# Kernel optimization log

Measured on AMD Instinct MI355X. Metric: run time of the kernel, lower is better.

## Reference

```python
import jax, jax.numpy as jnp
import numpy as np


def setup_inputs() -> dict:
    key = jax.random.key(0)
    ks = jax.random.split(key, 5)
    B, C, H, W = 32, 32, 64, 64   # latent feature map (latent_space_channel_dim=32)
    D, K = 32, 512                # quant_dim, codebook_size
    return {
        "z": jax.random.normal(ks[0], (B, C, H, W), jnp.float32),
        "quant_w": jax.random.normal(ks[1], (D, C), jnp.float32) * 0.1,   # 1x1 conv kernel
        "quant_b": jnp.zeros((D,), jnp.float32),
        "codebook": jax.random.normal(ks[2], (K, D), jnp.float32),
        "post_quant_w": jax.random.normal(ks[3], (C, D), jnp.float32) * 0.1,
        "post_quant_b": jnp.zeros((C,), jnp.float32),
    }


def reference(z, quant_w, quant_b, codebook, post_quant_w, post_quant_b):
    B, C, H, W = z.shape
    D = quant_w.shape[0]
    # quant_conv: 1x1 conv == channel GEMM
    x = jnp.einsum('bchw,dc->bdhw', z, quant_w) + quant_b[None, :, None, None]
    # rearrange 'b c h w -> b c (h w)' then flatten tokens to [B*HW, D]
    xf = x.transpose(0, 2, 3, 1).reshape(-1, D)
    # squared euclidean distances to codebook (cdist**2), argmin, gather
    d2 = (jnp.sum(xf * xf, axis=-1, keepdims=True)
          - 2.0 * (xf @ codebook.T)
          + jnp.sum(codebook * codebook, axis=-1)[None, :])  # [B*HW, K]
    idx = jnp.argmin(d2, axis=-1)                              # [B*HW]
    q = codebook[idx]                                          # gather [B*HW, D]
    # commitment loss (encoder pull) + codebook loss (learnable codebook, no EMA)
    commit = jnp.mean((jax.lax.stop_gradient(q) - xf) ** 2)
    cb_loss = jnp.mean((q - jax.lax.stop_gradient(xf)) ** 2)
    loss = commit + cb_loss
    # straight-through estimator
    q_st = xf + jax.lax.stop_gradient(q - xf)
    qmap = q_st.reshape(B, H, W, D).transpose(0, 3, 1, 2)      # 'b c (h w) -> b c h w'
    # post_quant_conv: 1x1 conv back to latent channels
    out = jnp.einsum('bdhw,cd->bchw', qmap, post_quant_w) + post_quant_b[None, :, None, None]
    return out, idx.reshape(B, H * W), loss
```

## Files before the change

### kernel.cpp

```cpp
#include <hip/hip_runtime.h>

#define C_    32
#define D_    32
#define K_    512
#define HW_   4096
#define NTOK  131072
#define IDX_OFF   4194304
#define LOSS_OFF  4325376
#define TAU   2e-4f

#define WS_CBN   0
#define WS_CBHF  4096
#define WS_CBLF  36864
#define WS_LOSSP 69632
#define WS_NEEDED 86016

typedef __attribute__((ext_vector_type(8))) _Float16 f16x8;
typedef __attribute__((ext_vector_type(8))) short    short8;
typedef __attribute__((ext_vector_type(4))) float    f32x4;

#define WAVE_FENCE() do { asm volatile("s_waitcnt lgkmcnt(0)" ::: "memory"); \
                          __builtin_amdgcn_sched_barrier(0); } while (0)

__device__ inline short f2h_hi(float v, float* rest) {
    const _Float16 h = (_Float16)v;
    *rest = v - (float)h;
    return __builtin_bit_cast(short, h);
}

__global__ __launch_bounds__(256)
void prep_cb(const float* __restrict__ cb, float* __restrict__ cbn,
             short* __restrict__ cbhf, short* __restrict__ cblf)
{
    const int k = blockIdx.x * 256 + threadIdx.x;
    const int nt = k >> 4, lr = k & 15;
    const float* row = cb + k * D_;
    float s = 0.f;
    short h[32], lo[32];
    #pragma unroll
    for (int d = 0; d < D_; ++d) {
        const float v = row[d]; s = fmaf(v, v, s);
        float r; h[d] = f2h_hi(v, &r);
        lo[d] = __builtin_bit_cast(short, (_Float16)r);
    }
    cbn[k] = s;
    #pragma unroll
    for (int j = 0; j < 4; ++j) {
        *(short8*)(cbhf + nt * 512 + (j * 16 + lr) * 8) = *(const short8*)(h  + 8 * j);
        *(short8*)(cblf + nt * 512 + (j * 16 + lr) * 8) = *(const short8*)(lo + 8 * j);
    }
}

__global__ __launch_bounds__(512, 2)
void vq_fused(const float* __restrict__ z,  const float* __restrict__ qw,
              const float* __restrict__ qb, const float* __restrict__ cb,
              const float* __restrict__ pw, const float* __restrict__ pb,
              const short* __restrict__ cbhf, const short* __restrict__ cblf,
              const float* __restrict__ cbn, float* __restrict__ lossp,
              float* __restrict__ out)
{
    __shared__ __align__(16) short cbh_s[16384];
    __shared__ __align__(16) short cbl_s[16384];
    __shared__ float cbn_s[K_];
    __shared__ float xsh[8][32][33];
    __shared__ int   sidx[8][32];

    const int tid = threadIdx.x;
    const int wv = tid >> 6, l = tid & 63;

    #pragma unroll
    for (int i = 0; i < 4; ++i)
        ((float4*)cbh_s)[tid + 512 * i] = ((const float4*)cbhf)[tid + 512 * i];
    #pragma unroll
    for (int i = 0; i < 4; ++i)
        ((float4*)cbl_s)[tid + 512 * i] = ((const float4*)cblf)[tid + 512 * i];
    if (tid < K_) cbn_s[tid] = cbn[tid];
    __syncthreads();

    const int T0 = (blockIdx.x * 8 + wv) * 32;
    const int b = T0 >> 12, hw0 = T0 & (HW_ - 1);
    const int tok = l & 31, half = l >> 5;

    {
        const float* zbase = z + (size_t)b * (C_ * HW_) + hw0 + tok;
        float zv[C_];
        #pragma unroll
        for (int c = 0; c < C_; ++c) zv[c] = zbase[(size_t)c * HW_];
        const int d0 = half * 16;
        #pragma unroll
        for (int i = 0; i < 16; ++i) {
            float a = qb[d0 + i];
            const float4* qr = (const float4*)(qw + (d0 + i) * C_);
            #pragma unroll
            for (int c4 = 0; c4 < 8; ++c4) {
                const float4 q4 = qr[c4];
                a = fmaf(zv[4*c4+0], q4.x, a); a = fmaf(zv[4*c4+1], q4.y, a);
                a = fmaf(zv[4*c4+2], q4.z, a); a = fmaf(zv[4*c4+3], q4.w, a);
            }
            xsh[wv][tok][d0 + i] = a;
        }
    }
    WAVE_FENCE();

    const int lr = l & 15, lg = l >> 4;
    short8 sh0, sl0, sh1, sl1;
    #pragma unroll
    for (int j = 0; j < 8; ++j) {
        float r0, r1;
        sh0[j] = f2h_hi(xsh[wv][lr][lg * 8 + j], &r0);
        sl0[j] = __builtin_bit_cast(short, (_Float16)r0);
        sh1[j] = f2h_hi(xsh[wv][16 + lr][lg * 8 + j], &r1);
        sl1[j] = __builtin_bit_cast(short, (_Float16)r1);
    }
    const f16x8 ah0 = __builtin_bit_cast(f16x8, sh0);
    const f16x8 al0 = __builtin_bit_cast(f16x8, sl0);
    const f16x8 ah1 = __builtin_bit_cast(f16x8, sh1);
    const f16x8 al1 = __builtin_bit_cast(f16x8, sl1);

    float b1[8], b2[8]; int i1[8];
    #pragma unroll
    for (int s = 0; s < 8; ++s) { b1[s] = 3.4e38f; b2[s] = 3.4e38f; i1[s] = 0; }

    #pragma unroll 2
    for (int nt = 0; nt < 32; ++nt) {
        const f16x8 bh = __builtin_bit_cast(f16x8, *(const short8*)(cbh_s + nt * 512 + l * 8));
        const f16x8 bl = __builtin_bit_cast(f16x8, *(const short8*)(cbl_s + nt * 512 + l * 8));
        const float cn = cbn_s[nt * 16 + lr];
        f32x4 acc0 = {0.f,0.f,0.f,0.f}, acc1 = {0.f,0.f,0.f,0.f};
        acc0 = __builtin_amdgcn_mfma_f32_16x16x32_f16(ah0, bh, acc0, 0, 0, 0);
        acc0 = __builtin_amdgcn_mfma_f32_16x16x32_f16(ah0, bl, acc0, 0, 0, 0);
        acc0 = __builtin_amdgcn_mfma_f32_16x16x32_f16(al0, bh, acc0, 0, 0, 0);
        acc1 = __builtin_amdgcn_mfma_f32_16x16x32_f16(ah1, bh, acc1, 0, 0, 0);
        acc1 = __builtin_amdgcn_mfma_f32_16x16x32_f16(ah1, bl, acc1, 0, 0, 0);
        acc1 = __builtin_amdgcn_mfma_f32_16x16x32_f16(al1, bh, acc1, 0, 0, 0);
        const int n = nt * 16 + lr;
        #pragma unroll
        for (int r = 0; r < 4; ++r) {
            {
                const float d2 = fmaf(-2.f, acc0[r], cn);
                const bool lt1 = d2 < b1[r], lt2 = d2 < b2[r];
                b2[r] = lt1 ? b1[r] : (lt2 ? d2 : b2[r]);
                b1[r] = lt1 ? d2 : b1[r];
                i1[r] = lt1 ? n  : i1[r];
            }
            {
                const float d2 = fmaf(-2.f, acc1[r], cn);
                const bool lt1 = d2 < b1[4+r], lt2 = d2 < b2[4+r];
                b2[4+r] = lt1 ? b1[4+r] : (lt2 ? d2 : b2[4+r]);
                b1[4+r] = lt1 ? d2 : b1[4+r];
                i1[4+r] = lt1 ? n  : i1[4+r];
            }
        }
    }
    #pragma unroll
    for (int mk = 1; mk < 16; mk <<= 1) {
        #pragma unroll
        for (int s = 0; s < 8; ++s) {
            const float ob1 = __shfl_xor(b1[s], mk);
            const int   oi1 = __shfl_xor(i1[s], mk);
            const float ob2 = __shfl_xor(b2[s], mk);
            const bool take = (ob1 < b1[s]) || (ob1 == b1[s] && oi1 < i1[s]);
            const float loser = take ? b1[s] : ob1;
            b1[s] = take ? ob1 : b1[s];
            i1[s] = take ? oi1 : i1[s];
            b2[s] = fminf(fminf(b2[s], ob2), loser);
        }
    }
    #pragma unroll
    for (int s = 0; s < 8; ++s) {
        if (lr == s) {
            const int tokW = (s >> 2) * 16 + lg * 4 + (s & 3);
            sidx[wv][tokW] = i1[s] | (((b2[s] - b1[s]) < TAU) ? 512 : 0);
        }
    }
    WAVE_FENCE();

    {
        const int sv = sidx[wv][tok];
        unsigned long long m = __ballot((l < 32) && (sv & 512));
        while (m) {
            const int j = __ffsll(m) - 1; m &= m - 1;
            float xfj[D_];
            #pragma unroll
            for (int d = 0; d < D_; ++d) xfj[d] = xsh[wv][j][d];
            float bb = 3.4e38f; int bi = 0;
            #pragma unroll
            for (int p = 0; p < 8; ++p) {
                const int c = l + 64 * p;
                const float* row = cb + (size_t)c * D_;
                float p0 = 0.f, p1 = 0.f, p2 = 0.f, p3 = 0.f;
                #pragma unroll
                for (int d = 0; d < D_; d += 4) {
                    p0 = fmaf(xfj[d],   row[d],   p0); p1 = fmaf(xfj[d+1], row[d+1], p1);
                    p2 = fmaf(xfj[d+2], row[d+2], p2); p3 = fmaf(xfj[d+3], row[d+3], p3);
                }
                const float dd = fmaf(-2.f, (p0 + p1) + (p2 + p3), cbn_s[c]);
                if (dd < bb) { bb = dd; bi = c; }
            }
            #pragma unroll
            for (int s = 1; s < 64; s <<= 1) {
                const float ob = __shfl_xor(bb, s); const int oi = __shfl_xor(bi, s);
                if (ob < bb || (ob == bb && oi < bi)) { bb = ob; bi = oi; }
            }
            if (l == j) sidx[wv][j] = bi;
        }
    }
    WAVE_FENCE();
    const int myidx = sidx[wv][tok] & 511;

    if (l < 32) out[IDX_OFF + T0 + l] = (float)(sidx[wv][l] & 511);

    float qreg[16];
    {
        const float4* qrow = (const float4*)(cb + (size_t)myidx * D_ + half * 16);
        #pragma unroll
        for (int d4 = 0; d4 < 4; ++d4) {
            const float4 t = qrow[d4];
            qreg[4*d4+0] = t.x; qreg[4*d4+1] = t.y; qreg[4*d4+2] = t.z; qreg[4*d4+3] = t.w;
        }
    }
    float lacc = 0.f;
    #pragma unroll
    for (int i = 0; i < 16; ++i) {
        const float df = qreg[i] - xsh[wv][tok][half * 16 + i];
        lacc = fmaf(df, df, lacc);
    }
    lacc += __shfl_down(lacc, 32);
    lacc += __shfl_down(lacc, 16); lacc += __shfl_down(lacc, 8);
    lacc += __shfl_down(lacc, 4);  lacc += __shfl_down(lacc, 2);
    lacc += __shfl_down(lacc, 1);
    if (l == 0) lossp[blockIdx.x * 8 + wv] = lacc;

    #pragma unroll
    for (int i = 0; i < 16; ++i) xsh[wv][tok][half * 16 + i] = qreg[i];
    WAVE_FENCE();

    {
        const int c0 = half * 16;
        float a[16];
        #pragma unroll
        for (int i = 0; i < 16; ++i) a[i] = pb[c0 + i];
        #pragma unroll
        for (int d4 = 0; d4 < 8; ++d4) {
            const float q0 = xsh[wv][tok][d4*4+0], q1 = xsh[wv][tok][d4*4+1];
            const float q2 = xsh[wv][tok][d4*4+2], q3 = xsh[wv][tok][d4*4+3];
            #pragma unroll
            for (int i = 0; i < 16; ++i) {
                const float4 p4 = *(const float4*)(pw + (c0 + i) * D_ + d4 * 4);
                a[i] = fmaf(q0, p4.x, a[i]); a[i] = fmaf(q1, p4.y, a[i]);
                a[i] = fmaf(q2, p4.z, a[i]); a[i] = fmaf(q3, p4.w, a[i]);
            }
        }
        float* obase = out + (size_t)b * (C_ * HW_) + hw0 + tok;
        #pragma unroll
        for (int i = 0; i < 16; ++i) obase[(size_t)(c0 + i) * HW_] = a[i];
    }
}

__global__ __launch_bounds__(256)
void loss_final(const float* __restrict__ lossp, float* __restrict__ out)
{
    __shared__ float lsum[4];
    const int tid = threadIdx.x;
    float s = 0.f;
    for (int i = tid; i < 4096; i += 256) s += lossp[i];
    s += __shfl_down(s, 32); s += __shfl_down(s, 16);
    s += __shfl_down(s, 8);  s += __shfl_down(s, 4);
    s += __shfl_down(s, 2);  s += __shfl_down(s, 1);
    const int wv = tid >> 6, l = tid & 63;
    if (l == 0) lsum[wv] = s;
    __syncthreads();
    if (tid == 0)
        out[LOSS_OFF] = ((lsum[0] + lsum[1]) + (lsum[2] + lsum[3])) * (2.0f / (float)(NTOK * D_));
}

__global__ __launch_bounds__(256)
void vq_mono(const float* __restrict__ z,  const float* __restrict__ qw,
             const float* __restrict__ qb, const float* __restrict__ cb,
             const float* __restrict__ pw, const float* __restrict__ pb,
             float* __restrict__ out)
{
    __shared__ float cbn_s[K_];
    __shared__ float lsum[4];
    const int tid = threadIdx.x;
    for (int k = tid; k < K_; k += 256) {
        const float* row = cb + k * D_;
        float s = 0.f;
        #pragma unroll
        for (int d = 0; d < D_; ++d) s = fmaf(row[d], row[d], s);
        cbn_s[k] = s;
    }
    __syncthreads();
    const int token = blockIdx.x * 256 + tid;
    const int b = token >> 12, hw = token & (HW_ - 1);
    const float* zbase = z + (size_t)b * C_ * HW_ + hw;
    float zv[C_];
    #pragma unroll
    for (int c = 0; c < C_; ++c) zv[c] = zbase[(size_t)c * HW_];
    float xf[D_];
    #pragma unroll
    for (int d = 0; d < D_; ++d) {
        float a = qb[d];
        #pragma unroll
        for (int c = 0; c < C_; ++c) a = fmaf(zv[c], qw[d * C_ + c], a);
        xf[d] = a;
    }
    float best = 3.4e38f; int bi = 0;
    #pragma unroll 2
    for (int k = 0; k < K_; ++k) {
        const float* row = cb + k * D_;
        float p0 = 0.f, p1 = 0.f, p2 = 0.f, p3 = 0.f;
        #pragma unroll
        for (int d = 0; d < D_; d += 4) {
            p0 = fmaf(xf[d+0], row[d+0], p0); p1 = fmaf(xf[d+1], row[d+1], p1);
            p2 = fmaf(xf[d+2], row[d+2], p2); p3 = fmaf(xf[d+3], row[d+3], p3);
        }
        const float s = fmaf(-2.f, (p0+p1)+(p2+p3), cbn_s[k]);
        if (s < best) { best = s; bi = k; }
    }
    out[IDX_OFF + token] = (float)bi;
    const float* qrow = cb + (size_t)bi * D_;
    float qv[D_];
    #pragma unroll
    for (int d = 0; d < D_; ++d) qv[d] = qrow[d];
    float l = 0.f;
    #pragma unroll
    for (int d = 0; d < D_; ++d) { const float df = qv[d] - xf[d]; l = fmaf(df, df, l); }
    float* obase = out + (size_t)b * C_ * HW_ + hw;
    #pragma unroll
    for (int c = 0; c < C_; ++c) {
        float a = pb[c];
        #pragma unroll
        for (int d = 0; d < D_; ++d) a = fmaf(qv[d], pw[c * D_ + d], a);
        obase[(size_t)c * HW_] = a;
    }
    #pragma unroll
    for (int off = 32; off; off >>= 1) l += __shfl_down(l, off);
    const int wid = tid >> 6, lane = tid & 63;
    if (lane == 0) lsum[wid] = l;
    __syncthreads();
    if (tid == 0) {
        const float t = (lsum[0] + lsum[1]) + (lsum[2] + lsum[3]);
        atomicAdd(out + LOSS_OFF, t * (2.0f / (float)(NTOK * D_)));
    }
}

extern "C" void kernel_launch(void* const* d_in, const int* in_sizes, int n_in,
                              void* d_out, int out_size, void* d_ws, size_t ws_size,
                              hipStream_t stream) {
    (void)in_sizes; (void)n_in; (void)out_size;
    const float* z  = (const float*)d_in[0];
    const float* qw = (const float*)d_in[1];
    const float* qb = (const float*)d_in[2];
    const float* cb = (const float*)d_in[3];
    const float* pw = (const float*)d_in[4];
    const float* pb = (const float*)d_in[5];
    float* out = (float*)d_out;

    if (ws_size < (size_t)WS_NEEDED) {
        hipMemsetAsync((char*)d_out + (size_t)LOSS_OFF * sizeof(float), 0, sizeof(float), stream);
        vq_mono<<<NTOK / 256, 256, 0, stream>>>(z, qw, qb, cb, pw, pb, out);
        return;
    }
    char* ws = (char*)d_ws;
    float* cbn   = (float*)(ws + WS_CBN);
    short* cbhf  = (short*)(ws + WS_CBHF);
    short* cblf  = (short*)(ws + WS_CBLF);
    float* lossp = (float*)(ws + WS_LOSSP);

    prep_cb<<<2, 256, 0, stream>>>(cb, cbn, cbhf, cblf);
    vq_fused<<<512, 512, 0, stream>>>(z, qw, qb, cb, pw, pb, cbhf, cblf, cbn, lossp, out);
    loss_final<<<1, 256, 0, stream>>>(lossp, out);
}
```

Measured before the change: 81.87 us.

## Keep projected tokens in MFMA register layout, pack argmin index into distance bits

The quant-conv output is now computed directly in the per-lane MFMA A-operand layout, so the xsh shared-memory staging buffer is dropped. Argmin tracking packs the candidate index into the low 9 mantissa bits of the distance and uses fminf/fmaxf, which removes the separate index registers and compares. Occupancy is raised to 4 blocks per CU, block IDs are swizzled, and the post-conv is restructured so each wave writes 64 contiguous tokens. The truncated distances force a much larger ambiguity threshold, which sends more tokens through the exact fp32 fallback path.

New measurement: 121.5 us. 1.48x slower.

```diff
diff --git a/kernel.cpp b/kernel.cpp
--- a/kernel.cpp
+++ b/kernel.cpp
@@ -7,7 +7,7 @@
 #define NTOK  131072
 #define IDX_OFF   4194304
 #define LOSS_OFF  4325376
-#define TAU   2e-4f
+#define TAU   1.6e-2f
 
 #define WS_CBN   0
 #define WS_CBHF  4096
@@ -21,12 +21,6 @@
 
 #define WAVE_FENCE() do { asm volatile("s_waitcnt lgkmcnt(0)" ::: "memory"); \
                           __builtin_amdgcn_sched_barrier(0); } while (0)
-
-__device__ inline short f2h_hi(float v, float* rest) {
-    const _Float16 h = (_Float16)v;
-    *rest = v - (float)h;
-    return __builtin_bit_cast(short, h);
-}
 
 __global__ __launch_bounds__(256)
 void prep_cb(const float* __restrict__ cb, float* __restrict__ cbn,
@@ -40,8 +34,9 @@
     #pragma unroll
     for (int d = 0; d < D_; ++d) {
         const float v = row[d]; s = fmaf(v, v, s);
-        float r; h[d] = f2h_hi(v, &r);
-        lo[d] = __builtin_bit_cast(short, (_Float16)r);
+        const _Float16 hh = (_Float16)v;
+        h[d]  = __builtin_bit_cast(short, hh);
+        lo[d] = __builtin_bit_cast(short, (_Float16)(v - (float)hh));
     }
     cbn[k] = s;
     #pragma unroll
@@ -51,7 +46,7 @@
     }
 }
 
-__global__ __launch_bounds__(512, 2)
+__global__ __launch_bounds__(512, 4)
 void vq_fused(const float* __restrict__ z,  const float* __restrict__ qw,
               const float* __restrict__ qb, const float* __restrict__ cb,
               const float* __restrict__ pw, const float* __restrict__ pb,
@@ -62,11 +57,11 @@
     __shared__ __align__(16) short cbh_s[16384];
     __shared__ __align__(16) short cbl_s[16384];
     __shared__ float cbn_s[K_];
-    __shared__ float xsh[8][32][33];
     __shared__ int   sidx[8][32];
 
     const int tid = threadIdx.x;
     const int wv = tid >> 6, l = tid & 63;
+    const int lr = l & 15, lg = l >> 4;
 
     #pragma unroll
     for (int i = 0; i < 4; ++i)
@@ -77,51 +72,56 @@
     if (tid < K_) cbn_s[tid] = cbn[tid];
     __syncthreads();
 
-    const int T0 = (blockIdx.x * 8 + wv) * 32;
+    const int bid = blockIdx.x;
+    const int swz = (bid & 7) * 64 + (bid >> 3);
+    const int T0 = swz * 256;
     const int b = T0 >> 12, hw0 = T0 & (HW_ - 1);
-    const int tok = l & 31, half = l >> 5;
-
+    const int hwW = hw0 + wv * 32;
+
+    float a0[8], a1[8];
     {
-        const float* zbase = z + (size_t)b * (C_ * HW_) + hw0 + tok;
-        float zv[C_];
-        #pragma unroll
-        for (int c = 0; c < C_; ++c) zv[c] = zbase[(size_t)c * HW_];
-        const int d0 = half * 16;
-        #pragma unroll
-        for (int i = 0; i < 16; ++i) {
-            float a = qb[d0 + i];
-            const float4* qr = (const float4*)(qw + (d0 + i) * C_);
-            #pragma unroll
-            for (int c4 = 0; c4 < 8; ++c4) {
-                const float4 q4 = qr[c4];
-                a = fmaf(zv[4*c4+0], q4.x, a); a = fmaf(zv[4*c4+1], q4.y, a);
-                a = fmaf(zv[4*c4+2], q4.z, a); a = fmaf(zv[4*c4+3], q4.w, a);
-            }
-            xsh[wv][tok][d0 + i] = a;
-        }
-    }
-    WAVE_FENCE();
-
-    const int lr = l & 15, lg = l >> 4;
+        const int d0 = lg * 8;
+        #pragma unroll
+        for (int j = 0; j < 8; ++j) { a0[j] = qb[d0 + j]; a1[j] = a0[j]; }
+        const float* z0 = z + (size_t)b * (C_ * HW_) + hwW + lr;
+        #pragma unroll
+        for (int c4 = 0; c4 < 8; ++c4) {
+            float z0v[4], z1v[4];
+            #pragma unroll
+            for (int u = 0; u < 4; ++u) {
+                z0v[u] = z0[(size_t)(c4 * 4 + u) * HW_];
+                z1v[u] = z0[(size_t)(c4 * 4 + u) * HW_ + 16];
+            }
+            #pragma unroll
+            for (int j = 0; j < 8; ++j) {
+                const float4 q4 = *(const float4*)(qw + (d0 + j) * C_ + c4 * 4);
+                a0[j] = fmaf(z0v[0], q4.x, a0[j]); a0[j] = fmaf(z0v[1], q4.y, a0[j]);
+                a0[j] = fmaf(z0v[2], q4.z, a0[j]); a0[j] = fmaf(z0v[3], q4.w, a0[j]);
+                a1[j] = fmaf(z1v[0], q4.x, a1[j]); a1[j] = fmaf(z1v[1], q4.y, a1[j]);
+                a1[j] = fmaf(z1v[2], q4.z, a1[j]); a1[j] = fmaf(z1v[3], q4.w, a1[j]);
+            }
+        }
+    }
     short8 sh0, sl0, sh1, sl1;
     #pragma unroll
     for (int j = 0; j < 8; ++j) {
-        float r0, r1;
-        sh0[j] = f2h_hi(xsh[wv][lr][lg * 8 + j], &r0);
-        sl0[j] = __builtin_bit_cast(short, (_Float16)r0);
-        sh1[j] = f2h_hi(xsh[wv][16 + lr][lg * 8 + j], &r1);
-        sl1[j] = __builtin_bit_cast(short, (_Float16)r1);
+        const _Float16 h0 = (_Float16)a0[j];
+        const _Float16 h1 = (_Float16)a1[j];
+        sh0[j] = __builtin_bit_cast(short, h0);
+        sl0[j] = __builtin_bit_cast(short, (_Float16)(a0[j] - (float)h0));
+        sh1[j] = __builtin_bit_cast(short, h1);
+        sl1[j] = __builtin_bit_cast(short, (_Float16)(a1[j] - (float)h1));
     }
     const f16x8 ah0 = __builtin_bit_cast(f16x8, sh0);
     const f16x8 al0 = __builtin_bit_cast(f16x8, sl0);
     const f16x8 ah1 = __builtin_bit_cast(f16x8, sh1);
     const f16x8 al1 = __builtin_bit_cast(f16x8, sl1);
 
-    float b1[8], b2[8]; int i1[8];
-    #pragma unroll
-    for (int s = 0; s < 8; ++s) { b1[s] = 3.4e38f; b2[s] = 3.4e38f; i1[s] = 0; }
-
-    #pragma unroll 2
+    float b1[8], b2[8];
+    #pragma unroll
+    for (int s = 0; s < 8; ++s) { b1[s] = 3.4e38f; b2[s] = 3.4e38f; }
+
+    #pragma unroll 4
     for (int nt = 0; nt < 32; ++nt) {
         const f16x8 bh = __builtin_bit_cast(f16x8, *(const short8*)(cbh_s + nt * 512 + l * 8));
         const f16x8 bl = __builtin_bit_cast(f16x8, *(const short8*)(cbl_s + nt * 512 + l * 8));
@@ -133,22 +133,22 @@
         acc1 = __builtin_amdgcn_mfma_f32_16x16x32_f16(ah1, bh, acc1, 0, 0, 0);
         acc1 = __builtin_amdgcn_mfma_f32_16x16x32_f16(ah1, bl, acc1, 0, 0, 0);
         acc1 = __builtin_amdgcn_mfma_f32_16x16x32_f16(al1, bh, acc1, 0, 0, 0);
-        const int n = nt * 16 + lr;
+        const unsigned nn = (unsigned)(nt * 16 + lr);
         #pragma unroll
         for (int r = 0; r < 4; ++r) {
             {
                 const float d2 = fmaf(-2.f, acc0[r], cn);
-                const bool lt1 = d2 < b1[r], lt2 = d2 < b2[r];
-                b2[r] = lt1 ? b1[r] : (lt2 ? d2 : b2[r]);
-                b1[r] = lt1 ? d2 : b1[r];
-                i1[r] = lt1 ? n  : i1[r];
+                const float k = __builtin_bit_cast(float,
+                    (__builtin_bit_cast(unsigned, d2) & 0xFFFFFE00u) | nn);
+                b2[r] = fminf(b2[r], fmaxf(k, b1[r]));
+                b1[r] = fminf(b1[r], k);
             }
             {
                 const float d2 = fmaf(-2.f, acc1[r], cn);
-                const bool lt1 = d2 < b1[4+r], lt2 = d2 < b2[4+r];
-                b2[4+r] = lt1 ? b1[4+r] : (lt2 ? d2 : b2[4+r]);
-                b1[4+r] = lt1 ? d2 : b1[4+r];
-                i1[4+r] = lt1 ? n  : i1[4+r];
+                const float k = __builtin_bit_cast(float,
+                    (__builtin_bit_cast(unsigned, d2) & 0xFFFFFE00u) | nn);
+                b2[4+r] = fminf(b2[4+r], fmaxf(k, b1[4+r]));
+                b1[4+r] = fminf(b1[4+r], k);
             }
         }
     }
@@ -156,33 +156,37 @@
     for (int mk = 1; mk < 16; mk <<= 1) {
         #pragma unroll
         for (int s = 0; s < 8; ++s) {
-            const float ob1 = __shfl_xor(b1[s], mk);
-            const int   oi1 = __shfl_xor(i1[s], mk);
-            const float ob2 = __shfl_xor(b2[s], mk);
-            const bool take = (ob1 < b1[s]) || (ob1 == b1[s] && oi1 < i1[s]);
-            const float loser = take ? b1[s] : ob1;
-            b1[s] = take ? ob1 : b1[s];
-            i1[s] = take ? oi1 : i1[s];
-            b2[s] = fminf(fminf(b2[s], ob2), loser);
+            const float o1 = __shfl_xor(b1[s], mk);
+            const float o2 = __shfl_xor(b2[s], mk);
+            b2[s] = fminf(fminf(b2[s], o2), fmaxf(b1[s], o1));
+            b1[s] = fminf(b1[s], o1);
         }
     }
     #pragma unroll
     for (int s = 0; s < 8; ++s) {
         if (lr == s) {
             const int tokW = (s >> 2) * 16 + lg * 4 + (s & 3);
-            sidx[wv][tokW] = i1[s] | (((b2[s] - b1[s]) < TAU) ? 512 : 0);
+            const int idx = (int)(__builtin_bit_cast(unsigned, b1[s]) & 511u);
+            sidx[wv][tokW] = idx | (((b2[s] - b1[s]) < TAU) ? 512 : 0);
         }
     }
     WAVE_FENCE();
 
     {
-        const int sv = sidx[wv][tok];
+        const int sv = sidx[wv][l & 31];
         unsigned long long m = __ballot((l < 32) && (sv & 512));
         while (m) {
             const int j = __ffsll(m) - 1; m &= m - 1;
             float xfj[D_];
-            #pragma unroll
-            for (int d = 0; d < D_; ++d) xfj[d] = xsh[wv][j][d];
+            if (j < 16) {
+                #pragma unroll
+                for (int d = 0; d < D_; ++d)
+                    xfj[d] = __shfl(a0[d & 7], (j & 15) + 16 * (d >> 3));
+            } else {
+                #pragma unroll
+                for (int d = 0; d < D_; ++d)
+                    xfj[d] = __shfl(a1[d & 7], (j & 15) + 16 * (d >> 3));
+            }
             float bb = 3.4e38f; int bi = 0;
             #pragma unroll
             for (int p = 0; p < 8; ++p) {
@@ -206,54 +210,64 @@
         }
     }
     WAVE_FENCE();
-    const int myidx = sidx[wv][tok] & 511;
-
-    if (l < 32) out[IDX_OFF + T0 + l] = (float)(sidx[wv][l] & 511);
-
-    float qreg[16];
+
     {
-        const float4* qrow = (const float4*)(cb + (size_t)myidx * D_ + half * 16);
-        #pragma unroll
-        for (int d4 = 0; d4 < 4; ++d4) {
+        const int i0 = sidx[wv][lr] & 511;
+        const int i1 = sidx[wv][16 + lr] & 511;
+        const int d0 = lg * 8;
+        const float4 qa = *(const float4*)(cb + (size_t)i0 * D_ + d0);
+        const float4 qb4 = *(const float4*)(cb + (size_t)i0 * D_ + d0 + 4);
+        const float4 qc = *(const float4*)(cb + (size_t)i1 * D_ + d0);
+        const float4 qd = *(const float4*)(cb + (size_t)i1 * D_ + d0 + 4);
+        float lacc = 0.f, df;
+        df = qa.x - a0[0]; lacc = fmaf(df, df, lacc);
+        df = qa.y - a0[1]; lacc = fmaf(df, df, lacc);
+        df = qa.z - a0[2]; lacc = fmaf(df, df, lacc);
+        df = qa.w - a0[3]; lacc = fmaf(df, df, lacc);
+        df = qb4.x - a0[4]; lacc = fmaf(df, df, lacc);
+        df = qb4.y - a0[5]; lacc = fmaf(df, df, lacc);
+        df = qb4.z - a0[6]; lacc = fmaf(df, df, lacc);
+        df = qb4.w - a0[7]; lacc = fmaf(df, df, lacc);
+        df = qc.x - a1[0]; lacc = fmaf(df, df, lacc);
+        df = qc.y - a1[1]; lacc = fmaf(df, df, lacc);
+        df = qc.z - a1[2]; lacc = fmaf(df, df, lacc);
+        df = qc.w - a1[3]; lacc = fmaf(df, df, lacc);
+        df = qd.x - a1[4]; lacc = fmaf(df, df, lacc);
+        df = qd.y - a1[5]; lacc = fmaf(df, df, lacc);
+        df = qd.z - a1[6]; lacc = fmaf(df, df, lacc);
+        df = qd.w - a1[7]; lacc = fmaf(df, df, lacc);
+        lacc += __shfl_down(lacc, 32); lacc += __shfl_down(lacc, 16);
+        lacc += __shfl_down(lacc, 8);  lacc += __shfl_down(lacc, 4);
+        lacc += __shfl_down(lacc, 2);  lacc += __shfl_down(lacc, 1);
+        if (l == 0) lossp[bid * 8 + wv] = lacc;
+    }
+    __syncthreads();
+
+    if (tid < 256) out[IDX_OFF + T0 + tid] = (float)(sidx[tid >> 5][tid & 31] & 511);
+
+    {
+        const int toff = (wv & 3) * 64 + l;
+        const int c0 = __builtin_amdgcn_readfirstlane(16 * (wv >> 2));
+        const int idxp = sidx[toff >> 5][toff & 31] & 511;
+        float qv[32];
+        const float4* qrow = (const float4*)(cb + (size_t)idxp * D_);
+        #pragma unroll
+        for (int d4 = 0; d4 < 8; ++d4) {
             const float4 t = qrow[d4];
-            qreg[4*d4+0] = t.x; qreg[4*d4+1] = t.y; qreg[4*d4+2] = t.z; qreg[4*d4+3] = t.w;
-        }
-    }
-    float lacc = 0.f;
-    #pragma unroll
-    for (int i = 0; i < 16; ++i) {
-        const float df = qreg[i] - xsh[wv][tok][half * 16 + i];
-        lacc = fmaf(df, df, lacc);
-    }
-    lacc += __shfl_down(lacc, 32);
-    lacc += __shfl_down(lacc, 16); lacc += __shfl_down(lacc, 8);
-    lacc += __shfl_down(lacc, 4);  lacc += __shfl_down(lacc, 2);
-    lacc += __shfl_down(lacc, 1);
-    if (l == 0) lossp[blockIdx.x * 8 + wv] = lacc;
-
-    #pragma unroll
-    for (int i = 0; i < 16; ++i) xsh[wv][tok][half * 16 + i] = qreg[i];
-    WAVE_FENCE();
-
-    {
-        const int c0 = half * 16;
-        float a[16];
-        #pragma unroll
-        for (int i = 0; i < 16; ++i) a[i] = pb[c0 + i];
-        #pragma unroll
-        for (int d4 = 0; d4 < 8; ++d4) {
-            const float q0 = xsh[wv][tok][d4*4+0], q1 = xsh[wv][tok][d4*4+1];
-            const float q2 = xsh[wv][tok][d4*4+2], q3 = xsh[wv][tok][d4*4+3];
-            #pragma unroll
-            for (int i = 0; i < 16; ++i) {
+            qv[4*d4+0] = t.x; qv[4*d4+1] = t.y; qv[4*d4+2] = t.z; qv[4*d4+3] = t.w;
+        }
+        float* obase = out + (size_t)b * (C_ * HW_) + hw0 + toff;
+        #pragma unroll
+        for (int i = 0; i < 16; ++i) {
+            float a = pb[c0 + i];
+            #pragma unroll
+            for (int d4 = 0; d4 < 8; ++d4) {
                 const float4 p4 = *(const float4*)(pw + (c0 + i) * D_ + d4 * 4);
-                a[i] = fmaf(q0, p4.x, a[i]); a[i] = fmaf(q1, p4.y, a[i]);
-                a[i] = fmaf(q2, p4.z, a[i]); a[i] = fmaf(q3, p4.w, a[i]);
-            }
-        }
-        float* obase = out + (size_t)b * (C_ * HW_) + hw0 + tok;
-        #pragma unroll
-        for (int i = 0; i < 16; ++i) obase[(size_t)(c0 + i) * HW_] = a[i];
+                a = fmaf(qv[4*d4+0], p4.x, a); a = fmaf(qv[4*d4+1], p4.y, a);
+                a = fmaf(qv[4*d4+2], p4.z, a); a = fmaf(qv[4*d4+3], p4.w, a);
+            }
+            obase[(size_t)(c0 + i) * HW_] = a;
+        }
     }
 }
 
```

## Drop xsh shared staging, keep projections in registers via cross-lane shuffles

Applied to the files above, without the earlier changes.

Removes the per-wave xsh shared-memory tile. The quant-conv outputs are now computed directly in the MFMA A-operand layout, with z values exchanged by lane shuffles, and fallback rows, loss and post-conv inputs are rebuilt from registers by shuffles. This cuts LDS use so that launch_bounds can ask for 4 blocks per CU instead of 2, raising occupancy. The cost is more shuffles, some duplicated codebook loads for the loss, and register pressure under the tighter bound, which could cause spills.

Result: slower. 84.71 us (+3.5%).

```diff
diff --git a/kernel.cpp b/kernel.cpp
--- a/kernel.cpp
+++ b/kernel.cpp
@@ -51,7 +51,7 @@
     }
 }
 
-__global__ __launch_bounds__(512, 2)
+__global__ __launch_bounds__(512, 4)
 void vq_fused(const float* __restrict__ z,  const float* __restrict__ qw,
               const float* __restrict__ qb, const float* __restrict__ cb,
               const float* __restrict__ pw, const float* __restrict__ pb,
@@ -62,11 +62,12 @@
     __shared__ __align__(16) short cbh_s[16384];
     __shared__ __align__(16) short cbl_s[16384];
     __shared__ float cbn_s[K_];
-    __shared__ float xsh[8][32][33];
     __shared__ int   sidx[8][32];
 
     const int tid = threadIdx.x;
     const int wv = tid >> 6, l = tid & 63;
+    const int lr = l & 15, lg = l >> 4;
+    const int tok = l & 31, half = l >> 5;
 
     #pragma unroll
     for (int i = 0; i < 4; ++i)
@@ -74,43 +75,50 @@
     #pragma unroll
     for (int i = 0; i < 4; ++i)
         ((float4*)cbl_s)[tid + 512 * i] = ((const float4*)cblf)[tid + 512 * i];
-    if (tid < K_) cbn_s[tid] = cbn[tid];
+    cbn_s[tid] = cbn[tid];
     __syncthreads();
 
     const int T0 = (blockIdx.x * 8 + wv) * 32;
     const int b = T0 >> 12, hw0 = T0 & (HW_ - 1);
-    const int tok = l & 31, half = l >> 5;
-
+
+    float a0[8], a1[8];
     {
         const float* zbase = z + (size_t)b * (C_ * HW_) + hw0 + tok;
         float zv[C_];
         #pragma unroll
         for (int c = 0; c < C_; ++c) zv[c] = zbase[(size_t)c * HW_];
-        const int d0 = half * 16;
-        #pragma unroll
-        for (int i = 0; i < 16; ++i) {
-            float a = qb[d0 + i];
-            const float4* qr = (const float4*)(qw + (d0 + i) * C_);
+
+        const int d0 = lg * 8;
+        #pragma unroll
+        for (int j = 0; j < 8; ++j) { a0[j] = qb[d0 + j]; a1[j] = a0[j]; }
+
+        const int podd = lg & 1;
+        #pragma unroll
+        for (int c4 = 0; c4 < 8; ++c4) {
+            float zA[4], zB[4];
             #pragma unroll
-            for (int c4 = 0; c4 < 8; ++c4) {
-                const float4 q4 = qr[c4];
-                a = fmaf(zv[4*c4+0], q4.x, a); a = fmaf(zv[4*c4+1], q4.y, a);
-                a = fmaf(zv[4*c4+2], q4.z, a); a = fmaf(zv[4*c4+3], q4.w, a);
-            }
-            xsh[wv][tok][d0 + i] = a;
-        }
-    }
-    WAVE_FENCE();
-
-    const int lr = l & 15, lg = l >> 4;
+            for (int u = 0; u < 4; ++u) {
+                const float zo = __shfl_xor(zv[c4 * 4 + u], 16);
+                zA[u] = podd ? zo : zv[c4 * 4 + u];
+                zB[u] = podd ? zv[c4 * 4 + u] : zo;
+            }
+            #pragma unroll
+            for (int j = 0; j < 8; ++j) {
+                const float4 q4 = *(const float4*)(qw + (d0 + j) * C_ + c4 * 4);
+                a0[j] = fmaf(zA[0], q4.x, a0[j]); a0[j] = fmaf(zA[1], q4.y, a0[j]);
+                a0[j] = fmaf(zA[2], q4.z, a0[j]); a0[j] = fmaf(zA[3], q4.w, a0[j]);
+                a1[j] = fmaf(zB[0], q4.x, a1[j]); a1[j] = fmaf(zB[1], q4.y, a1[j]);
+                a1[j] = fmaf(zB[2], q4.z, a1[j]); a1[j] = fmaf(zB[3], q4.w, a1[j]);
+            }
+        }
+    }
+
     short8 sh0, sl0, sh1, sl1;
     #pragma unroll
     for (int j = 0; j < 8; ++j) {
         float r0, r1;
-        sh0[j] = f2h_hi(xsh[wv][lr][lg * 8 + j], &r0);
-        sl0[j] = __builtin_bit_cast(short, (_Float16)r0);
-        sh1[j] = f2h_hi(xsh[wv][16 + lr][lg * 8 + j], &r1);
-        sl1[j] = __builtin_bit_cast(short, (_Float16)r1);
+        sh0[j] = f2h_hi(a0[j], &r0); sl0[j] = __builtin_bit_cast(short, (_Float16)r0);
+        sh1[j] = f2h_hi(a1[j], &r1); sl1[j] = __builtin_bit_cast(short, (_Float16)r1);
     }
     const f16x8 ah0 = __builtin_bit_cast(f16x8, sh0);
     const f16x8 al0 = __builtin_bit_cast(f16x8, sl0);
@@ -181,8 +189,15 @@
         while (m) {
             const int j = __ffsll(m) - 1; m &= m - 1;
             float xfj[D_];
-            #pragma unroll
-            for (int d = 0; d < D_; ++d) xfj[d] = xsh[wv][j][d];
+            if (j < 16) {
+                #pragma unroll
+                for (int d = 0; d < D_; ++d)
+                    xfj[d] = __shfl(a0[d & 7], (j & 15) + 16 * (d >> 3));
+            } else {
+                #pragma unroll
+                for (int d = 0; d < D_; ++d)
+                    xfj[d] = __shfl(a1[d & 7], (j & 15) + 16 * (d >> 3));
+            }
             float bb = 3.4e38f; int bi = 0;
             #pragma unroll
             for (int p = 0; p < 8; ++p) {
@@ -210,40 +225,53 @@
 
     if (l < 32) out[IDX_OFF + T0 + l] = (float)(sidx[wv][l] & 511);
 
-    float qreg[16];
     {
+        const int d0 = lg * 8;
+        const int iA = sidx[wv][lr] & 511;
+        const int iB = sidx[wv][16 + lr] & 511;
+        const float4 qa = *(const float4*)(cb + (size_t)iA * D_ + d0);
+        const float4 qa2 = *(const float4*)(cb + (size_t)iA * D_ + d0 + 4);
+        const float4 qc = *(const float4*)(cb + (size_t)iB * D_ + d0);
+        const float4 qc2 = *(const float4*)(cb + (size_t)iB * D_ + d0 + 4);
+        float qA[8] = {qa.x, qa.y, qa.z, qa.w, qa2.x, qa2.y, qa2.z, qa2.w};
+        float qB[8] = {qc.x, qc.y, qc.z, qc.w, qc2.x, qc2.y, qc2.z, qc2.w};
+        float lacc = 0.f;
+        #pragma unroll
+        for (int j = 0; j < 8; ++j) {
+            const float dA = qA[j] - a0[j], dB = qB[j] - a1[j];
+            lacc = fmaf(dA, dA, lacc); lacc = fmaf(dB, dB, lacc);
+        }
+        lacc += __shfl_down(lacc, 32); lacc += __shfl_down(lacc, 16);
+        lacc += __shfl_down(lacc, 8);  lacc += __shfl_down(lacc, 4);
+        lacc += __shfl_down(lacc, 2);  lacc += __shfl_down(lacc, 1);
+        if (l == 0) lossp[blockIdx.x * 8 + wv] = lacc;
+    }
+
+    {
+        float qreg[16];
         const float4* qrow = (const float4*)(cb + (size_t)myidx * D_ + half * 16);
         #pragma unroll
         for (int d4 = 0; d4 < 4; ++d4) {
             const float4 t = qrow[d4];
             qreg[4*d4+0] = t.x; qreg[4*d4+1] = t.y; qreg[4*d4+2] = t.z; qreg[4*d4+3] = t.w;
         }
-    }
-    float lacc = 0.f;
-    #pragma unroll
-    for (int i = 0; i < 16; ++i) {
-        const float df = qreg[i] - xsh[wv][tok][half * 16 + i];
-        lacc = fmaf(df, df, lacc);
-    }
-    lacc += __shfl_down(lacc, 32);
-    lacc += __shfl_down(lacc, 16); lacc += __shfl_down(lacc, 8);
-    lacc += __shfl_down(lacc, 4);  lacc += __shfl_down(lacc, 2);
-    lacc += __shfl_down(lacc, 1);
-    if (l == 0) lossp[blockIdx.x * 8 + wv] = lacc;
-
-    #pragma unroll
-    for (int i = 0; i < 16; ++i) xsh[wv][tok][half * 16 + i] = qreg[i];
-    WAVE_FENCE();
-
-    {
+        float qlo[16], qhi[16];
+        #pragma unroll
+        for (int i = 0; i < 16; ++i) {
+            const float qo = __shfl_xor(qreg[i], 32);
+            qlo[i] = half ? qo : qreg[i];
+            qhi[i] = half ? qreg[i] : qo;
+        }
         const int c0 = half * 16;
         float a[16];
         #pragma unroll
         for (int i = 0; i < 16; ++i) a[i] = pb[c0 + i];
         #pragma unroll
         for (int d4 = 0; d4 < 8; ++d4) {
-            const float q0 = xsh[wv][tok][d4*4+0], q1 = xsh[wv][tok][d4*4+1];
-            const float q2 = xsh[wv][tok][d4*4+2], q3 = xsh[wv][tok][d4*4+3];
+            const float q0 = (d4 < 4) ? qlo[d4*4+0] : qhi[(d4-4)*4+0];
+            const float q1 = (d4 < 4) ? qlo[d4*4+1] : qhi[(d4-4)*4+1];
+            const float q2 = (d4 < 4) ? qlo[d4*4+2] : qhi[(d4-4)*4+2];
+            const float q3 = (d4 < 4) ? qlo[d4*4+3] : qhi[(d4-4)*4+3];
             #pragma unroll
             for (int i = 0; i < 16; ++i) {
                 const float4 p4 = *(const float4*)(pw + (c0 + i) * D_ + d4 * 4);
```
